# Kernel tuning notes

Measured on AMD Instinct MI355X. Metric: run time of the kernel, lower is better.

## Reference

```python
import jax, jax.numpy as jnp
import numpy as np

B, S, D, H, F = 4, 1024, 1024, 16, 4096
DH = D // H
EPS = 1e-6


def _layer_norm(x, gamma, beta):
    # torch LayerNorm here uses unbiased std (ddof=1) and eps added to std
    mean = jnp.mean(x, axis=-1, keepdims=True)
    std = jnp.std(x, axis=-1, keepdims=True, ddof=1)
    return gamma * (x - mean) / (std + EPS) + beta


def _conv1d(x, w, b):
    # x: [B,S,C]; w: [out,in,3]; pad 'both' -> (1,1), same length
    y = jax.lax.conv_general_dilated(
        jnp.transpose(x, (0, 2, 1)), w, window_strides=(1,),
        padding=[(1, 1)], dimension_numbers=('NCH', 'OIH', 'NCH'))
    return jnp.transpose(y, (0, 2, 1)) + b


def setup_inputs() -> dict:
    key = jax.random.key(0)
    ks = jax.random.split(key, 8)
    sD = 1.0 / np.sqrt(D)
    sF = 1.0 / np.sqrt(F)
    return {
        'inputs': jax.random.normal(ks[0], (B, S, D), dtype=jnp.float32),
        'mask': jnp.zeros((B, 1, S), dtype=bool),
        'gamma1': jnp.ones((D,), jnp.float32),
        'beta1': jnp.zeros((D,), jnp.float32),
        'gamma2': jnp.ones((D,), jnp.float32),
        'beta2': jnp.zeros((D,), jnp.float32),
        'Wq': jax.random.normal(ks[1], (D, D), jnp.float32) * sD,
        'Wk': jax.random.normal(ks[2], (D, D), jnp.float32) * sD,
        'Wv': jax.random.normal(ks[3], (D, D), jnp.float32) * sD,
        'Wo': jax.random.normal(ks[4], (D, D), jnp.float32) * sD,
        'conv1_w': jax.random.normal(ks[5], (F, D, 3), jnp.float32) * sD,
        'conv1_b': jnp.zeros((F,), jnp.float32),
        'conv2_w': jax.random.normal(ks[6], (D, F, 3), jnp.float32) * sF,
        'conv2_b': jnp.zeros((D,), jnp.float32),
    }


def reference(inputs, mask, gamma1, beta1, gamma2, beta2, Wq, Wk, Wv, Wo,
              conv1_w, conv1_b, conv2_w, conv2_b):
    x = inputs
    x_norm = _layer_norm(x, gamma1, beta1)
    # projections (torch Linear, no bias): y = x @ W.T
    q = jnp.einsum('bsd,ed->bse', x_norm, Wq).reshape(B, S, H, DH).transpose(0, 2, 1, 3)
    k = jnp.einsum('bsd,ed->bse', x_norm, Wk).reshape(B, S, H, DH).transpose(0, 2, 1, 3)
    v = jnp.einsum('bsd,ed->bse', x_norm, Wv).reshape(B, S, H, DH).transpose(0, 2, 1, 3)
    q = q * (DH ** -0.5)
    logits = jnp.einsum('bhqd,bhkd->bhqk', q, k)  # [B,H,S,S]
    logits = jnp.where(mask[:, None, :, :], jnp.float32(-1e18), logits)
    weights = jax.nn.softmax(logits, axis=-1)
    ctx = jnp.einsum('bhqk,bhkd->bhqd', weights, v)
    ctx = ctx.transpose(0, 2, 1, 3).reshape(B, S, D)
    attn_out = jnp.einsum('bsd,ed->bse', ctx, Wo)
    x = x + attn_out  # layer dropout is identity at eval
    x_norm = _layer_norm(x, gamma2, beta2)
    # FFN 'cc': conv+relu applied after BOTH convs (source bug i<len always true)
    h = jax.nn.relu(_conv1d(x_norm, conv1_w, conv1_b))
    h = jax.nn.relu(_conv1d(h, conv2_w, conv2_b))
    return x + h
```

## Files before the change

kernel.cpp:

```cpp
#include <hip/hip_runtime.h>
#include <stdint.h>
#include <stddef.h>

typedef unsigned short u16;
typedef short short8 __attribute__((ext_vector_type(8)));
typedef float f32x4 __attribute__((ext_vector_type(4)));

#define B_ 4
#define S_ 1024
#define D_ 1024
#define H_ 16
#define F_ 4096
#define M_ 4096

__device__ __forceinline__ u16 f2bf(float f) {
  union { float f; unsigned u; } v; v.f = f;
  unsigned r = v.u + 0x7fffu + ((v.u >> 16) & 1u);
  return (u16)(r >> 16);
}
__device__ __forceinline__ float bf2f(u16 x) {
  union { unsigned u; float f; } v; v.u = ((unsigned)x) << 16; return v.f;
}

__device__ __forceinline__ void gld16(const u16* g, u16* l) {
  __builtin_amdgcn_global_load_lds(
      (__attribute__((address_space(1))) void*)g,
      (__attribute__((address_space(3))) void*)l, 16, 0, 0);
}

__global__ __launch_bounds__(256) void cvt_wqkvo(const float* __restrict__ q,
                                                 const float* __restrict__ k,
                                                 const float* __restrict__ v,
                                                 const float* __restrict__ o,
                                                 u16* __restrict__ d) {
  int i = blockIdx.x * 256 + threadIdx.x;
  int sel = i >> 18;
  const float* s = sel == 0 ? q : sel == 1 ? k : sel == 2 ? v : o;
  float sc = sel == 0 ? 0.125f : 1.0f;
  float4 val = *(const float4*)(s + (size_t)(i & 262143) * 4);
  unsigned lo = (unsigned)f2bf(val.x * sc) | ((unsigned)f2bf(val.y * sc) << 16);
  unsigned hi = (unsigned)f2bf(val.z * sc) | ((unsigned)f2bf(val.w * sc) << 16);
  *(uint2*)(d + (size_t)i * 4) = make_uint2(lo, hi);
}

__global__ __launch_bounds__(256) void pack3(const float* __restrict__ w,
                                             u16* __restrict__ d, int OUT, int IN) {
  int tot = OUT * IN;
  int i = blockIdx.x * blockDim.x + threadIdx.x;
  int stride = gridDim.x * blockDim.x;
  for (; i < tot; i += stride) {
#pragma unroll
    for (int t = 0; t < 3; ++t) d[(size_t)t * tot + i] = f2bf(w[(size_t)i * 3 + t]);
  }
}

__global__ __launch_bounds__(256) void layernorm(const float* __restrict__ x,
                                                 const float* __restrict__ g,
                                                 const float* __restrict__ be,
                                                 u16* __restrict__ out) {
  __shared__ float red[8];
  const int row = blockIdx.x, tid = threadIdx.x;
  const float* xr = x + (size_t)row * D_;
  float4 v = *(const float4*)(xr + tid * 4);
  float s = v.x + v.y + v.z + v.w;
  float q = v.x * v.x + v.y * v.y + v.z * v.z + v.w * v.w;
#pragma unroll
  for (int o = 32; o; o >>= 1) { s += __shfl_xor(s, o); q += __shfl_xor(q, o); }
  const int w = tid >> 6, lane = tid & 63;
  if (lane == 0) { red[w] = s; red[4 + w] = q; }
  __syncthreads();
  s = red[0] + red[1] + red[2] + red[3];
  q = red[4] + red[5] + red[6] + red[7];
  float mean = s * (1.f / 1024.f);
  float var = (q - 1024.f * mean * mean) * (1.f / 1023.f);
  var = fmaxf(var, 0.f);
  float r = 1.f / (sqrtf(var) + 1e-6f);
  const float* vv = &v.x;
  int c = tid * 4;
  unsigned lo = (unsigned)f2bf(g[c + 0] * (vv[0] - mean) * r + be[c + 0]) |
                ((unsigned)f2bf(g[c + 1] * (vv[1] - mean) * r + be[c + 1]) << 16);
  unsigned hi = (unsigned)f2bf(g[c + 2] * (vv[2] - mean) * r + be[c + 2]) |
                ((unsigned)f2bf(g[c + 3] * (vv[3] - mean) * r + be[c + 3]) << 16);
  *(uint2*)(out + (size_t)row * D_ + c) = make_uint2(lo, hi);
}

template <int EPI, int NXB>
__global__ __launch_bounds__(256) void gemm_bt(const u16* __restrict__ A,
                                               const u16* __restrict__ Bm,
                                               int N, int K,
                                               void* __restrict__ C,
                                               const float* __restrict__ res) {
  __shared__ u16 As[128 * 64];
  __shared__ u16 Bs[128 * 64];
  const int tid = threadIdx.x;
  const int w = tid >> 6, lane = tid & 63;
  const int bid = blockIdx.x;
  const int idx = bid >> 3;
  const int xb = (bid & 7) * NXB + idx % NXB;
  const int yb = idx / NXB;
  const int m0 = yb * 128, n0 = xb * 128;
  const int wr = w >> 1, wc = w & 1;
  const int lrow = lane >> 3;
  const int swc = (lane & 7) ^ lrow;

  f32x4 acc[4][4] = {};

  for (int k0 = 0; k0 < K; k0 += 64) {
#pragma unroll
    for (int i = 0; i < 4; ++i) {
      int chunk = w * 4 + i;
      int row = chunk * 8 + lrow;
      gld16(A + (size_t)(m0 + row) * K + k0 + swc * 8, &As[chunk * 512]);
      gld16(Bm + (size_t)(n0 + row) * K + k0 + swc * 8, &Bs[chunk * 512]);
    }
    __syncthreads();
#pragma unroll
    for (int kk = 0; kk < 2; ++kk) {
      short8 aF[4], bF[4];
#pragma unroll
      for (int mi = 0; mi < 4; ++mi) {
        int row = wr * 64 + mi * 16 + (lane & 15);
        int ch = (kk * 4 + (lane >> 4)) ^ (row & 7);
        aF[mi] = *(const short8*)&As[row * 64 + ch * 8];
      }
#pragma unroll
      for (int ni = 0; ni < 4; ++ni) {
        int row = wc * 64 + ni * 16 + (lane & 15);
        int ch = (kk * 4 + (lane >> 4)) ^ (row & 7);
        bF[ni] = *(const short8*)&Bs[row * 64 + ch * 8];
      }
#pragma unroll
      for (int mi = 0; mi < 4; ++mi)
#pragma unroll
        for (int ni = 0; ni < 4; ++ni)
          acc[mi][ni] = __builtin_amdgcn_mfma_f32_16x16x32_bf16(aF[mi], bF[ni], acc[mi][ni], 0, 0, 0);
    }
    __syncthreads();
  }

#pragma unroll
  for (int mi = 0; mi < 4; ++mi)
#pragma unroll
    for (int ni = 0; ni < 4; ++ni)
#pragma unroll
      for (int j = 0; j < 4; ++j) {
        int row = m0 + wr * 64 + mi * 16 + (lane >> 4) * 4 + j;
        int col = n0 + wc * 64 + ni * 16 + (lane & 15);
        float v = acc[mi][ni][j];
        if (EPI == 0) ((u16*)C)[(size_t)row * N + col] = f2bf(v);
        else ((float*)C)[(size_t)row * N + col] = v + res[(size_t)row * N + col];
      }
}

__global__ __launch_bounds__(256) void conv1_gemm(const u16* __restrict__ A,
                                                  const u16* __restrict__ Bm,
                                                  const float* __restrict__ bias,
                                                  const u16* __restrict__ zrow,
                                                  u16* __restrict__ Cb) {
  const int K = 1024, N = 4096;
  __shared__ u16 As[128 * 64];
  __shared__ u16 Bs[128 * 64];
  const int tid = threadIdx.x;
  const int w = tid >> 6, lane = tid & 63;
  const int bid = blockIdx.x;
  const int idx = bid >> 3;
  const int xb = (bid & 7) * 4 + (idx & 3);
  const int yb = idx >> 2;
  const int m0 = yb * 128, n0 = xb * 128;
  const int bb = m0 >> 10, s0 = m0 & 1023;
  const int wr = w >> 1, wc = w & 1;
  const int lrow = lane >> 3;
  const int swc = (lane & 7) ^ lrow;

  f32x4 acc[4][4] = {};

  for (int t = 0; t < 3; ++t) {
    const u16* Bt = Bm + (size_t)t * N * K;
    for (int k0 = 0; k0 < K; k0 += 64) {
#pragma unroll
      for (int i = 0; i < 4; ++i) {
        int chunk = w * 4 + i;
        int row = chunk * 8 + lrow;
        int s = s0 + row + t - 1;
        const u16* asrc = ((unsigned)s < 1024u)
                              ? A + (size_t)(bb * 1024 + s) * K + k0 + swc * 8
                              : zrow + k0 + swc * 8;
        gld16(asrc, &As[chunk * 512]);
        gld16(Bt + (size_t)(n0 + row) * K + k0 + swc * 8, &Bs[chunk * 512]);
      }
      __syncthreads();
#pragma unroll
      for (int kk = 0; kk < 2; ++kk) {
        short8 aF[4], bF[4];
#pragma unroll
        for (int mi = 0; mi < 4; ++mi) {
          int row = wr * 64 + mi * 16 + (lane & 15);
          int ch = (kk * 4 + (lane >> 4)) ^ (row & 7);
          aF[mi] = *(const short8*)&As[row * 64 + ch * 8];
        }
#pragma unroll
        for (int ni = 0; ni < 4; ++ni) {
          int row = wc * 64 + ni * 16 + (lane & 15);
          int ch = (kk * 4 + (lane >> 4)) ^ (row & 7);
          bF[ni] = *(const short8*)&Bs[row * 64 + ch * 8];
        }
#pragma unroll
        for (int mi = 0; mi < 4; ++mi)
#pragma unroll
          for (int ni = 0; ni < 4; ++ni)
            acc[mi][ni] = __builtin_amdgcn_mfma_f32_16x16x32_bf16(aF[mi], bF[ni], acc[mi][ni], 0, 0, 0);
      }
      __syncthreads();
    }
  }

#pragma unroll
  for (int mi = 0; mi < 4; ++mi)
#pragma unroll
    for (int ni = 0; ni < 4; ++ni)
#pragma unroll
      for (int j = 0; j < 4; ++j) {
        int rl = wr * 64 + mi * 16 + (lane >> 4) * 4 + j;
        int col = n0 + wc * 64 + ni * 16 + (lane & 15);
        float v = fmaxf(acc[mi][ni][j] + bias[col], 0.f);
        Cb[(size_t)(m0 + rl) * N + col] = f2bf(v);
      }
}

__global__ __launch_bounds__(256) void conv2_tap(const u16* __restrict__ A,
                                                 const u16* __restrict__ Bm,
                                                 const u16* __restrict__ zrow,
                                                 u16* __restrict__ P) {
  const int K = 4096, N = 1024;
  __shared__ u16 As[128 * 64];
  __shared__ u16 Bs[128 * 64];
  const int tid = threadIdx.x;
  const int w = tid >> 6, lane = tid & 63;
  const int bid = blockIdx.x;
  const int idx = bid >> 3;
  const int t = idx % 3;
  const int yb = idx / 3;
  const int xb = bid & 7;
  const int m0 = yb * 128, n0 = xb * 128;
  const int bb = m0 >> 10, s0 = m0 & 1023;
  const int wr = w >> 1, wc = w & 1;
  const int lrow = lane >> 3;
  const int swc = (lane & 7) ^ lrow;

  f32x4 acc[4][4] = {};
  const u16* Bt = Bm + (size_t)t * N * K;

  for (int k0 = 0; k0 < K; k0 += 64) {
#pragma unroll
    for (int i = 0; i < 4; ++i) {
      int chunk = w * 4 + i;
      int row = chunk * 8 + lrow;
      int s = s0 + row + t - 1;
      const u16* asrc = ((unsigned)s < 1024u)
                            ? A + (size_t)(bb * 1024 + s) * K + k0 + swc * 8
                            : zrow + k0 + swc * 8;
      gld16(asrc, &As[chunk * 512]);
      gld16(Bt + (size_t)(n0 + row) * K + k0 + swc * 8, &Bs[chunk * 512]);
    }
    __syncthreads();
#pragma unroll
    for (int kk = 0; kk < 2; ++kk) {
      short8 aF[4], bF[4];
#pragma unroll
      for (int mi = 0; mi < 4; ++mi) {
        int row = wr * 64 + mi * 16 + (lane & 15);
        int ch = (kk * 4 + (lane >> 4)) ^ (row & 7);
        aF[mi] = *(const short8*)&As[row * 64 + ch * 8];
      }
#pragma unroll
      for (int ni = 0; ni < 4; ++ni) {
        int row = wc * 64 + ni * 16 + (lane & 15);
        int ch = (kk * 4 + (lane >> 4)) ^ (row & 7);
        bF[ni] = *(const short8*)&Bs[row * 64 + ch * 8];
      }
#pragma unroll
      for (int mi = 0; mi < 4; ++mi)
#pragma unroll
        for (int ni = 0; ni < 4; ++ni)
          acc[mi][ni] = __builtin_amdgcn_mfma_f32_16x16x32_bf16(aF[mi], bF[ni], acc[mi][ni], 0, 0, 0);
    }
    __syncthreads();
  }

#pragma unroll
  for (int mi = 0; mi < 4; ++mi)
#pragma unroll
    for (int ni = 0; ni < 4; ++ni)
#pragma unroll
      for (int j = 0; j < 4; ++j) {
        int rl = wr * 64 + mi * 16 + (lane >> 4) * 4 + j;
        int col = n0 + wc * 64 + ni * 16 + (lane & 15);
        P[((size_t)t * 4096 + m0 + rl) * 1024 + col] = f2bf(acc[mi][ni][j]);
      }
}

__global__ __launch_bounds__(256) void conv2_reduce(const u16* __restrict__ P,
                                                    const float* __restrict__ bias,
                                                    const float* __restrict__ x2,
                                                    float* __restrict__ out) {
  size_t o = ((size_t)blockIdx.x * 256 + threadIdx.x) * 8;
  int col = (int)(o & 1023);
  short8 a = *(const short8*)(P + o);
  short8 b = *(const short8*)(P + 4194304 + o);
  short8 c = *(const short8*)(P + 8388608 + o);
  float4 r0 = *(const float4*)(x2 + o);
  float4 r1 = *(const float4*)(x2 + o + 4);
  float4 b0 = *(const float4*)(bias + col);
  float4 b1 = *(const float4*)(bias + col + 4);
  float4 o0, o1;
  const float* bb0 = &b0.x; const float* bb1 = &b1.x;
  float* p0 = &o0.x; float* p1 = &o1.x;
  const float* rr0 = &r0.x; const float* rr1 = &r1.x;
#pragma unroll
  for (int j = 0; j < 4; ++j) {
    float v = bf2f((u16)a[j]) + bf2f((u16)b[j]) + bf2f((u16)c[j]) + bb0[j];
    p0[j] = rr0[j] + fmaxf(v, 0.f);
  }
#pragma unroll
  for (int j = 0; j < 4; ++j) {
    float v = bf2f((u16)a[4 + j]) + bf2f((u16)b[4 + j]) + bf2f((u16)c[4 + j]) + bb1[j];
    p1[j] = rr1[j] + fmaxf(v, 0.f);
  }
  *(float4*)(out + o) = o0;
  *(float4*)(out + o + 4) = o1;
}

__global__ __launch_bounds__(256) void transpose_v(const u16* __restrict__ QKV,
                                                   u16* __restrict__ Vt) {
  __shared__ u16 T[64][72];
  const int tid = threadIdx.x;
  const int st = blockIdx.x, h = blockIdx.y, b = blockIdx.z;
  const int s0 = st * 64;
#pragma unroll
  for (int i = 0; i < 2; ++i) {
    int u = tid + i * 256;
    int s = u >> 3, c8 = u & 7;
    uint4 val = *(const uint4*)(QKV + (size_t)(b * 1024 + s0 + s) * 3072 + 2048 + h * 64 + c8 * 8);
    const u16* vp = (const u16*)&val;
#pragma unroll
    for (int k = 0; k < 8; ++k) T[s][c8 * 8 + k] = vp[k];
  }
  __syncthreads();
#pragma unroll
  for (int i = 0; i < 2; ++i) {
    int u = tid + i * 256;
    int d = u >> 3, c8 = u & 7;
    u16 tmp[8];
#pragma unroll
    for (int k = 0; k < 8; ++k) tmp[k] = T[c8 * 8 + k][d];
    uint4 o;
    o.x = (unsigned)tmp[0] | ((unsigned)tmp[1] << 16);
    o.y = (unsigned)tmp[2] | ((unsigned)tmp[3] << 16);
    o.z = (unsigned)tmp[4] | ((unsigned)tmp[5] << 16);
    o.w = (unsigned)tmp[6] | ((unsigned)tmp[7] << 16);
    *(uint4*)(Vt + (size_t)((b * 16 + h) * 64 + d) * 1024 + s0 + c8 * 8) = o;
  }
}

__global__ __launch_bounds__(256) void flash_attn(const u16* __restrict__ QKV,
                                                  const u16* __restrict__ Vt,
                                                  u16* __restrict__ Ctx) {
  __shared__ u16 Ks[64 * 64];
  __shared__ u16 Vs[64 * 64];
  __shared__ u16 Ps[4 * 16 * 64];
  const int tid = threadIdx.x;
  const int w = tid >> 6, lane = tid & 63;
  const int qt = blockIdx.x, h = blockIdx.y, b = blockIdx.z;
  const int q0 = qt * 64 + w * 16;
  const int lrow = lane >> 3;
  const int swc = (lane & 7) ^ lrow;

  short8 qF[2];
#pragma unroll
  for (int kk = 0; kk < 2; ++kk)
    qF[kk] = *(const short8*)(QKV + (size_t)(b * 1024 + q0 + (lane & 15)) * 3072 +
                              h * 64 + kk * 32 + (lane >> 4) * 8);

  float m_r[4], l_r[4];
  f32x4 accO[4] = {};
#pragma unroll
  for (int j = 0; j < 4; ++j) { m_r[j] = -1e30f; l_r[j] = 0.f; }

  for (int kt = 0; kt < 16; ++kt) {
#pragma unroll
    for (int i = 0; i < 2; ++i) {
      int chunk = w * 2 + i;
      int row = chunk * 8 + lrow;
      gld16(QKV + (size_t)(b * 1024 + kt * 64 + row) * 3072 + 1024 + h * 64 + swc * 8,
            &Ks[chunk * 512]);
      gld16(Vt + (size_t)((b * 16 + h) * 64 + row) * 1024 + kt * 64 + swc * 8, &Vs[chunk * 512]);
    }
    __syncthreads();

    f32x4 accS[4] = {};
#pragma unroll
    for (int nt = 0; nt < 4; ++nt) {
#pragma unroll
      for (int kk = 0; kk < 2; ++kk) {
        int row = nt * 16 + (lane & 15);
        int ch = (kk * 4 + (lane >> 4)) ^ (row & 7);
        short8 bF = *(const short8*)&Ks[row * 64 + ch * 8];
        accS[nt] = __builtin_amdgcn_mfma_f32_16x16x32_bf16(qF[kk], bF, accS[nt], 0, 0, 0);
      }
    }

#pragma unroll
    for (int j = 0; j < 4; ++j) {
      float mx = fmaxf(fmaxf(accS[0][j], accS[1][j]), fmaxf(accS[2][j], accS[3][j]));
#pragma unroll
      for (int o = 1; o < 16; o <<= 1) mx = fmaxf(mx, __shfl_xor(mx, o));
      float mnew = fmaxf(m_r[j], mx);
      int prow = (lane >> 4) * 4 + j;
      float s = 0.f;
#pragma unroll
      for (int nt = 0; nt < 4; ++nt) {
        float p = __expf(accS[nt][j] - mnew);
        s += p;
        int col = nt * 16 + (lane & 15);
        int ch = (col >> 3) ^ (prow & 7);
        Ps[w * 1024 + prow * 64 + ch * 8 + (col & 7)] = f2bf(p);
      }
#pragma unroll
      for (int o = 1; o < 16; o <<= 1) s += __shfl_xor(s, o);
      float alpha = __expf(m_r[j] - mnew);
      l_r[j] = l_r[j] * alpha + s;
      m_r[j] = mnew;
#pragma unroll
      for (int nt = 0; nt < 4; ++nt) accO[nt][j] *= alpha;
    }

#pragma unroll
    for (int kk = 0; kk < 2; ++kk) {
      int prow = lane & 15;
      int ch = (kk * 4 + (lane >> 4)) ^ (prow & 7);
      short8 aF = *(const short8*)&Ps[w * 1024 + prow * 64 + ch * 8];
#pragma unroll
      for (int nt = 0; nt < 4; ++nt) {
        int vrow = nt * 16 + (lane & 15);
        int vch = (kk * 4 + (lane >> 4)) ^ (vrow & 7);
        short8 bF = *(const short8*)&Vs[vrow * 64 + vch * 8];
        accO[nt] = __builtin_amdgcn_mfma_f32_16x16x32_bf16(aF, bF, accO[nt], 0, 0, 0);
      }
    }
    __syncthreads();
  }

#pragma unroll
  for (int nt = 0; nt < 4; ++nt)
#pragma unroll
    for (int j = 0; j < 4; ++j) {
      int row = q0 + (lane >> 4) * 4 + j;
      int col = h * 64 + nt * 16 + (lane & 15);
      Ctx[(size_t)(b * 1024 + row) * D_ + col] = f2bf(accO[nt][j] / l_r[j]);
    }
}

extern "C" void kernel_launch(void* const* d_in, const int* in_sizes, int n_in,
                              void* d_out, int out_size, void* d_ws, size_t ws_size,
                              hipStream_t stream) {
  const float* x_in = (const float*)d_in[0];
  const float* g1 = (const float*)d_in[2];
  const float* be1 = (const float*)d_in[3];
  const float* g2 = (const float*)d_in[4];
  const float* be2 = (const float*)d_in[5];
  const float* Wq = (const float*)d_in[6];
  const float* Wk = (const float*)d_in[7];
  const float* Wv = (const float*)d_in[8];
  const float* Wo = (const float*)d_in[9];
  const float* c1w = (const float*)d_in[10];
  const float* c1b = (const float*)d_in[11];
  const float* c2w = (const float*)d_in[12];
  const float* c2b = (const float*)d_in[13];
  float* out = (float*)d_out;
  char* ws = (char*)d_ws;

  const size_t OFF_WQKV = 0;
  const size_t OFF_WOB  = 6291456;
  const size_t OFF_W1T  = 8388608;
  const size_t OFF_W2T  = 33554432;
  const size_t OFF_XN1  = 58720256;
  const size_t OFF_QKV  = 67108864;
  const size_t OFF_H    = OFF_QKV;
  const size_t OFF_VT   = 100663296;
  const size_t OFF_X2   = 109051904;
  const size_t OFF_XN2  = 125829120;
  const size_t OFF_ZROW = 134217728;
  const size_t OFF_P    = 0;
  const size_t NEED     = 134225920;
  if (ws_size < NEED) return;

  u16* wqkv = (u16*)(ws + OFF_WQKV);
  u16* wo_b = (u16*)(ws + OFF_WOB);
  u16* w1t = (u16*)(ws + OFF_W1T);
  u16* w2t = (u16*)(ws + OFF_W2T);
  u16* xn1 = (u16*)(ws + OFF_XN1);
  u16* ctx = xn1;
  u16* qkv = (u16*)(ws + OFF_QKV);
  u16* hbuf = (u16*)(ws + OFF_H);
  u16* vt = (u16*)(ws + OFF_VT);
  float* x2 = (float*)(ws + OFF_X2);
  u16* xn2 = (u16*)(ws + OFF_XN2);
  u16* zrow = (u16*)(ws + OFF_ZROW);
  u16* part = (u16*)(ws + OFF_P);

  hipMemsetAsync(zrow, 0, 8192, stream);

  cvt_wqkvo<<<4096, 256, 0, stream>>>(Wq, Wk, Wv, Wo, wqkv);
  pack3<<<2048, 256, 0, stream>>>(c1w, w1t, F_, D_);
  pack3<<<2048, 256, 0, stream>>>(c2w, w2t, D_, F_);

  layernorm<<<M_, 256, 0, stream>>>(x_in, g1, be1, xn1);

  gemm_bt<0, 3><<<768, 256, 0, stream>>>(xn1, wqkv, 3072, 1024, qkv, nullptr);

  transpose_v<<<dim3(16, H_, B_), 256, 0, stream>>>(qkv, vt);

  flash_attn<<<dim3(16, H_, B_), 256, 0, stream>>>(qkv, vt, ctx);

  gemm_bt<1, 1><<<256, 256, 0, stream>>>(ctx, wo_b, 1024, 1024, x2, x_in);

  layernorm<<<M_, 256, 0, stream>>>(x2, g2, be2, xn2);

  conv1_gemm<<<1024, 256, 0, stream>>>(xn2, w1t, c1b, zrow, hbuf);

  conv2_tap<<<768, 256, 0, stream>>>(hbuf, w2t, zrow, part);
  conv2_reduce<<<2048, 256, 0, stream>>>(part, c2b, x2, out);
}
```

Measured before the change: 417.4 us.

## Replace 128x128 GEMMs with double-buffered 256x256 pipelined MFMA kernel

Introduces a templated gemm256 kernel with 256x256 tiles, 512 threads, double-buffered LDS and staged global-to-LDS prefetch interleaved with MFMA phases, using s_setprio and explicit waitcnt control. It replaces the QKV projection, conv1 and conv2-tap kernels. The aim is to raise arithmetic intensity per tile and hide global load latency behind compute. Larger tiles mean fewer blocks (192-256) on a chip with many CUs, which risks poor occupancy and wave quantization, and the explicit vmcnt/barrier scheduling adds correctness risk.

Measured after the change: 408.0 us. 1.02x faster.

```diff
diff --git a/kernel.cpp b/kernel.cpp
--- a/kernel.cpp
+++ b/kernel.cpp
@@ -82,6 +82,148 @@
   unsigned hi = (unsigned)f2bf(g[c + 2] * (vv[2] - mean) * r + be[c + 2]) |
                 ((unsigned)f2bf(g[c + 3] * (vv[3] - mean) * r + be[c + 3]) << 16);
   *(uint2*)(out + (size_t)row * D_ + c) = make_uint2(lo, hi);
+}
+
+template <int MODE, int NN, int KK>
+__device__ __forceinline__ void stage_half(int kt, int kind, const u16* __restrict__ Ag,
+                                           const u16* __restrict__ Bg,
+                                           const u16* __restrict__ zrow, int tapf,
+                                           int m0, int n0, int tid,
+                                           u16* AsB, u16* BsB) {
+  const int buf = kt & 1;
+  int tap, k0;
+  if (MODE == 1) { tap = kt >> 4; k0 = (kt & 15) << 6; }
+  else if (MODE == 2) { tap = tapf; k0 = kt << 6; }
+  else { tap = 0; k0 = kt << 6; }
+  const int gc = (tid & 7) ^ ((tid >> 3) & 7);
+  if (kind < 2) {
+#pragma unroll
+    for (int j = 0; j < 2; ++j) {
+      int r = kind * 64 + j * 128 + (tid >> 3);
+      const u16* src;
+      if (MODE == 0) {
+        src = Ag + (size_t)(m0 + r) * KK + k0 + gc * 8;
+      } else {
+        int srow = (m0 & 1023) + r + tap - 1;
+        src = ((unsigned)srow < 1024u)
+                  ? Ag + (size_t)((m0 & ~1023) + srow) * KK + k0 + gc * 8
+                  : zrow + k0 + gc * 8;
+      }
+      gld16(src, AsB + buf * 16384 + r * 64 + (tid & 7) * 8);
+    }
+  } else {
+#pragma unroll
+    for (int j = 0; j < 2; ++j) {
+      int r = (kind - 2) * 128 + j * 64 + (tid >> 3);
+      const u16* src = Bg + (size_t)tap * NN * KK + (size_t)(n0 + r) * KK + k0 + gc * 8;
+      gld16(src, BsB + buf * 16384 + r * 64 + (tid & 7) * 8);
+    }
+  }
+}
+
+template <int MODE, int NN, int KK, int NT>
+__global__ __launch_bounds__(512, 2) void gemm256(const u16* __restrict__ Ag,
+                                                  const u16* __restrict__ Bg,
+                                                  const float* __restrict__ bias,
+                                                  const u16* __restrict__ zrow,
+                                                  u16* __restrict__ Cb) {
+  __shared__ u16 As[2][256][64];
+  __shared__ u16 Bs[2][256][64];
+  const int tid = threadIdx.x;
+  const int w = tid >> 6, lane = tid & 63;
+  const int wr = w >> 2, wc = w & 3;
+
+  const int bid = blockIdx.x;
+  int wgid, mb, nb, tapf = 0;
+  if (MODE == 1) wgid = (bid & 7) * 32 + (bid >> 3);
+  else           wgid = (bid & 7) * 24 + (bid >> 3);
+  if (MODE == 2) {
+    mb = wgid & 15;
+    int rest = wgid >> 4;
+    tapf = rest >> 2;
+    nb = rest & 3;
+  } else {
+    nb = wgid >> 4;
+    mb = wgid & 15;
+  }
+  const int m0 = mb * 256, n0 = nb * 256;
+
+  u16* AsB = &As[0][0][0];
+  u16* BsB = &Bs[0][0][0];
+
+  f32x4 acc[8][4] = {};
+
+  stage_half<MODE, NN, KK>(0, 0, Ag, Bg, zrow, tapf, m0, n0, tid, AsB, BsB);
+  stage_half<MODE, NN, KK>(0, 1, Ag, Bg, zrow, tapf, m0, n0, tid, AsB, BsB);
+  stage_half<MODE, NN, KK>(0, 2, Ag, Bg, zrow, tapf, m0, n0, tid, AsB, BsB);
+  stage_half<MODE, NN, KK>(0, 3, Ag, Bg, zrow, tapf, m0, n0, tid, AsB, BsB);
+  stage_half<MODE, NN, KK>(1, 0, Ag, Bg, zrow, tapf, m0, n0, tid, AsB, BsB);
+  asm volatile("s_waitcnt vmcnt(2)" ::: "memory");
+  __builtin_amdgcn_s_barrier();
+
+  for (int kt = 0; kt < NT; ++kt) {
+    const int buf = kt & 1;
+#pragma unroll
+    for (int q = 0; q < 4; ++q) {
+      short8 aF[2][2], bF[4][2];
+#pragma unroll
+      for (int i = 0; i < 2; ++i)
+#pragma unroll
+        for (int kk = 0; kk < 2; ++kk) {
+          int r = wr * 128 + (2 * q + i) * 16 + (lane & 15);
+          int c = kk * 4 + (lane >> 4);
+          aF[i][kk] = *(const short8*)&As[buf][r][(c ^ (r & 7)) * 8];
+        }
+#pragma unroll
+      for (int ni = 0; ni < 4; ++ni)
+#pragma unroll
+        for (int kk = 0; kk < 2; ++kk) {
+          int r = wc * 64 + ni * 16 + (lane & 15);
+          int c = kk * 4 + (lane >> 4);
+          bF[ni][kk] = *(const short8*)&Bs[buf][r][(c ^ (r & 7)) * 8];
+        }
+      if (q == 0) { if (kt + 1 < NT) stage_half<MODE, NN, KK>(kt + 1, 1, Ag, Bg, zrow, tapf, m0, n0, tid, AsB, BsB); }
+      else if (q == 1) { if (kt + 1 < NT) stage_half<MODE, NN, KK>(kt + 1, 2, Ag, Bg, zrow, tapf, m0, n0, tid, AsB, BsB); }
+      else if (q == 2) { if (kt + 1 < NT) stage_half<MODE, NN, KK>(kt + 1, 3, Ag, Bg, zrow, tapf, m0, n0, tid, AsB, BsB); }
+      else {
+        if (kt + 2 < NT) stage_half<MODE, NN, KK>(kt + 2, 0, Ag, Bg, zrow, tapf, m0, n0, tid, AsB, BsB);
+        if (kt + 2 < NT)      asm volatile("s_waitcnt vmcnt(2)" ::: "memory");
+        else if (kt + 1 < NT) asm volatile("s_waitcnt vmcnt(0)" ::: "memory");
+      }
+      __builtin_amdgcn_s_barrier();
+      asm volatile("s_waitcnt lgkmcnt(0)" ::: "memory");
+      __builtin_amdgcn_sched_barrier(0);
+      __builtin_amdgcn_s_setprio(1);
+#pragma unroll
+      for (int i = 0; i < 2; ++i)
+#pragma unroll
+        for (int ni = 0; ni < 4; ++ni)
+#pragma unroll
+          for (int kk = 0; kk < 2; ++kk)
+            acc[2 * q + i][ni] = __builtin_amdgcn_mfma_f32_16x16x32_bf16(
+                aF[i][kk], bF[ni][kk], acc[2 * q + i][ni], 0, 0, 0);
+      __builtin_amdgcn_s_setprio(0);
+      __builtin_amdgcn_s_barrier();
+    }
+  }
+
+#pragma unroll
+  for (int mi = 0; mi < 8; ++mi)
+#pragma unroll
+    for (int ni = 0; ni < 4; ++ni)
+#pragma unroll
+      for (int j = 0; j < 4; ++j) {
+        int row = m0 + wr * 128 + mi * 16 + (lane >> 4) * 4 + j;
+        int col = n0 + wc * 64 + ni * 16 + (lane & 15);
+        float v = acc[mi][ni][j];
+        if (MODE == 0) {
+          Cb[(size_t)row * NN + col] = f2bf(v);
+        } else if (MODE == 1) {
+          Cb[(size_t)row * NN + col] = f2bf(fmaxf(v + bias[col], 0.f));
+        } else {
+          Cb[((size_t)tapf * 4096 + row) * NN + col] = f2bf(v);
+        }
+      }
 }
 
 template <int EPI, int NXB>
@@ -152,153 +294,6 @@
       }
 }
 
-__global__ __launch_bounds__(256) void conv1_gemm(const u16* __restrict__ A,
-                                                  const u16* __restrict__ Bm,
-                                                  const float* __restrict__ bias,
-                                                  const u16* __restrict__ zrow,
-                                                  u16* __restrict__ Cb) {
-  const int K = 1024, N = 4096;
-  __shared__ u16 As[128 * 64];
-  __shared__ u16 Bs[128 * 64];
-  const int tid = threadIdx.x;
-  const int w = tid >> 6, lane = tid & 63;
-  const int bid = blockIdx.x;
-  const int idx = bid >> 3;
-  const int xb = (bid & 7) * 4 + (idx & 3);
-  const int yb = idx >> 2;
-  const int m0 = yb * 128, n0 = xb * 128;
-  const int bb = m0 >> 10, s0 = m0 & 1023;
-  const int wr = w >> 1, wc = w & 1;
-  const int lrow = lane >> 3;
-  const int swc = (lane & 7) ^ lrow;
-
-  f32x4 acc[4][4] = {};
-
-  for (int t = 0; t < 3; ++t) {
-    const u16* Bt = Bm + (size_t)t * N * K;
-    for (int k0 = 0; k0 < K; k0 += 64) {
-#pragma unroll
-      for (int i = 0; i < 4; ++i) {
-        int chunk = w * 4 + i;
-        int row = chunk * 8 + lrow;
-        int s = s0 + row + t - 1;
-        const u16* asrc = ((unsigned)s < 1024u)
-                              ? A + (size_t)(bb * 1024 + s) * K + k0 + swc * 8
-                              : zrow + k0 + swc * 8;
-        gld16(asrc, &As[chunk * 512]);
-        gld16(Bt + (size_t)(n0 + row) * K + k0 + swc * 8, &Bs[chunk * 512]);
-      }
-      __syncthreads();
-#pragma unroll
-      for (int kk = 0; kk < 2; ++kk) {
-        short8 aF[4], bF[4];
-#pragma unroll
-        for (int mi = 0; mi < 4; ++mi) {
-          int row = wr * 64 + mi * 16 + (lane & 15);
-          int ch = (kk * 4 + (lane >> 4)) ^ (row & 7);
-          aF[mi] = *(const short8*)&As[row * 64 + ch * 8];
-        }
-#pragma unroll
-        for (int ni = 0; ni < 4; ++ni) {
-          int row = wc * 64 + ni * 16 + (lane & 15);
-          int ch = (kk * 4 + (lane >> 4)) ^ (row & 7);
-          bF[ni] = *(const short8*)&Bs[row * 64 + ch * 8];
-        }
-#pragma unroll
-        for (int mi = 0; mi < 4; ++mi)
-#pragma unroll
-          for (int ni = 0; ni < 4; ++ni)
-            acc[mi][ni] = __builtin_amdgcn_mfma_f32_16x16x32_bf16(aF[mi], bF[ni], acc[mi][ni], 0, 0, 0);
-      }
-      __syncthreads();
-    }
-  }
-
-#pragma unroll
-  for (int mi = 0; mi < 4; ++mi)
-#pragma unroll
-    for (int ni = 0; ni < 4; ++ni)
-#pragma unroll
-      for (int j = 0; j < 4; ++j) {
-        int rl = wr * 64 + mi * 16 + (lane >> 4) * 4 + j;
-        int col = n0 + wc * 64 + ni * 16 + (lane & 15);
-        float v = fmaxf(acc[mi][ni][j] + bias[col], 0.f);
-        Cb[(size_t)(m0 + rl) * N + col] = f2bf(v);
-      }
-}
-
-__global__ __launch_bounds__(256) void conv2_tap(const u16* __restrict__ A,
-                                                 const u16* __restrict__ Bm,
-                                                 const u16* __restrict__ zrow,
-                                                 u16* __restrict__ P) {
-  const int K = 4096, N = 1024;
-  __shared__ u16 As[128 * 64];
-  __shared__ u16 Bs[128 * 64];
-  const int tid = threadIdx.x;
-  const int w = tid >> 6, lane = tid & 63;
-  const int bid = blockIdx.x;
-  const int idx = bid >> 3;
-  const int t = idx % 3;
-  const int yb = idx / 3;
-  const int xb = bid & 7;
-  const int m0 = yb * 128, n0 = xb * 128;
-  const int bb = m0 >> 10, s0 = m0 & 1023;
-  const int wr = w >> 1, wc = w & 1;
-  const int lrow = lane >> 3;
-  const int swc = (lane & 7) ^ lrow;
-
-  f32x4 acc[4][4] = {};
-  const u16* Bt = Bm + (size_t)t * N * K;
-
-  for (int k0 = 0; k0 < K; k0 += 64) {
-#pragma unroll
-    for (int i = 0; i < 4; ++i) {
-      int chunk = w * 4 + i;
-      int row = chunk * 8 + lrow;
-      int s = s0 + row + t - 1;
-      const u16* asrc = ((unsigned)s < 1024u)
-                            ? A + (size_t)(bb * 1024 + s) * K + k0 + swc * 8
-                            : zrow + k0 + swc * 8;
-      gld16(asrc, &As[chunk * 512]);
-      gld16(Bt + (size_t)(n0 + row) * K + k0 + swc * 8, &Bs[chunk * 512]);
-    }
-    __syncthreads();
-#pragma unroll
-    for (int kk = 0; kk < 2; ++kk) {
-      short8 aF[4], bF[4];
-#pragma unroll
-      for (int mi = 0; mi < 4; ++mi) {
-        int row = wr * 64 + mi * 16 + (lane & 15);
-        int ch = (kk * 4 + (lane >> 4)) ^ (row & 7);
-        aF[mi] = *(const short8*)&As[row * 64 + ch * 8];
-      }
-#pragma unroll
-      for (int ni = 0; ni < 4; ++ni) {
-        int row = wc * 64 + ni * 16 + (lane & 15);
-        int ch = (kk * 4 + (lane >> 4)) ^ (row & 7);
-        bF[ni] = *(const short8*)&Bs[row * 64 + ch * 8];
-      }
-#pragma unroll
-      for (int mi = 0; mi < 4; ++mi)
-#pragma unroll
-        for (int ni = 0; ni < 4; ++ni)
-          acc[mi][ni] = __builtin_amdgcn_mfma_f32_16x16x32_bf16(aF[mi], bF[ni], acc[mi][ni], 0, 0, 0);
-    }
-    __syncthreads();
-  }
-
-#pragma unroll
-  for (int mi = 0; mi < 4; ++mi)
-#pragma unroll
-    for (int ni = 0; ni < 4; ++ni)
-#pragma unroll
-      for (int j = 0; j < 4; ++j) {
-        int rl = wr * 64 + mi * 16 + (lane >> 4) * 4 + j;
-        int col = n0 + wc * 64 + ni * 16 + (lane & 15);
-        P[((size_t)t * 4096 + m0 + rl) * 1024 + col] = f2bf(acc[mi][ni][j]);
-      }
-}
-
 __global__ __launch_bounds__(256) void conv2_reduce(const u16* __restrict__ P,
                                                     const float* __restrict__ bias,
                                                     const float* __restrict__ x2,
@@ -516,7 +511,7 @@
 
   layernorm<<<M_, 256, 0, stream>>>(x_in, g1, be1, xn1);
 
-  gemm_bt<0, 3><<<768, 256, 0, stream>>>(xn1, wqkv, 3072, 1024, qkv, nullptr);
+  gemm256<0, 3072, 1024, 16><<<192, 512, 0, stream>>>(xn1, wqkv, nullptr, zrow, qkv);
 
   transpose_v<<<dim3(16, H_, B_), 256, 0, stream>>>(qkv, vt);
 
@@ -526,8 +521,8 @@
 
   layernorm<<<M_, 256, 0, stream>>>(x2, g2, be2, xn2);
 
-  conv1_gemm<<<1024, 256, 0, stream>>>(xn2, w1t, c1b, zrow, hbuf);
-
-  conv2_tap<<<768, 256, 0, stream>>>(hbuf, w2t, zrow, part);
+  gemm256<1, 4096, 1024, 48><<<256, 512, 0, stream>>>(xn2, w1t, c1b, zrow, hbuf);
+
+  gemm256<2, 1024, 4096, 64><<<192, 512, 0, stream>>>(hbuf, w2t, nullptr, zrow, part);
   conv2_reduce<<<2048, 256, 0, stream>>>(part, c2b, x2, out);
 }
```
